# Performance work log

Hardware: AMD Instinct MI355X
Metric: run time of the kernel (lower is better)

The kernel has to match this reference:

```python
import jax, jax.numpy as jnp
import numpy as np

N, C, H, W = 64, 64, 128, 128
KH, KW = 3, 3


def setup_inputs() -> dict:
    key = jax.random.key(0)
    k1, k2 = jax.random.split(key)
    images = jax.random.normal(k1, (N, C, H, W), dtype=jnp.float32)
    kernels = jax.random.normal(k2, (N, C, KH, KW), dtype=jnp.float32)
    return {"images": images, "kernels": kernels}


def reference(images, kernels):
    # Per-sample conv: image i ([C,H,W]) convolved with kernel i ([C,kh,kw]) -> 1 channel.
    # Equivalent to a grouped conv with N groups:
    #   input  [1, N*C, H, W], weights [N, C, kh, kw], feature_group_count=N
    n, c, h, w = images.shape
    x = images.reshape(1, n * c, h, w)
    out = jax.lax.conv_general_dilated(
        x, kernels,
        window_strides=(1, 1),
        padding='VALID',
        dimension_numbers=('NCHW', 'OIHW', 'NCHW'),
        feature_group_count=n,
    )  # [1, N, H', W']
    return out.reshape(n, 1, out.shape[2], out.shape[3])
```

## Files before the change

kernel.cpp:

```cpp
#include <hip/hip_runtime.h>


#define NS   64
#define CCH  64
#define HH   128
#define WW   128
#define OHH  126
#define OWW  126
#define TH   16
#define IR   18
#define LDW  132
#define LDW4 33

__global__ __launch_bounds__(256, 2)
void ImageWiseConv2d_kernel(const float* __restrict__ img,
                            const float* __restrict__ ker,
                            float* __restrict__ out)
{
    __shared__ float buf[2][IR * LDW];

    const int tid = threadIdx.x;
    const int bx  = blockIdx.x;
    const int n   = bx >> 3;
    const int bt  = bx & 7;
    const int h0  = bt * TH;

    const int tx32 = tid & 31;
    const int rb   = tid >> 5;
    const float4* img4 = (const float4*)img;
    int gbase = (n * CCH) * (HH * WW / 4) + (h0 + rb) * (WW / 4) + tx32;
    const bool w2 = (rb < 2);
    const bool g2 = w2 && (h0 + rb + 16 < HH);
    const int lw0 = rb * LDW4 + tx32;

    const int tx = tid & 31;
    const int ty = tid >> 5;
    const int r0 = 2 * ty;
    const int c0 = 4 * tx;

    float acc0[4] = {0.f, 0.f, 0.f, 0.f};
    float acc1[4] = {0.f, 0.f, 0.f, 0.f};

    {
        float4 p0 = img4[gbase];
        float4 p1 = img4[gbase + 8 * (WW / 4)];
        float4 p2 = g2 ? img4[gbase + 16 * (WW / 4)] : make_float4(0.f, 0.f, 0.f, 0.f);
        float4* b0 = (float4*)buf[0];
        b0[lw0] = p0;
        b0[lw0 + 8 * LDW4] = p1;
        if (w2) b0[lw0 + 16 * LDW4] = p2;
    }
    __syncthreads();

    const float* __restrict__ kb = ker + (n * CCH) * 9;

    for (int c = 0; c < CCH; ++c) {
        float4 p0, p1, p2;
        const bool more = (c + 1 < CCH);
        if (more) {
            int gb = gbase + (c + 1) * (HH * WW / 4);
            p0 = img4[gb];
            p1 = img4[gb + 8 * (WW / 4)];
            p2 = g2 ? img4[gb + 16 * (WW / 4)] : make_float4(0.f, 0.f, 0.f, 0.f);
        }

        float w[9];
        #pragma unroll
        for (int q = 0; q < 9; ++q) w[q] = kb[c * 9 + q];

        const float* bc = buf[c & 1];
        float f[4][8];
        #pragma unroll
        for (int r = 0; r < 4; ++r) {
            float4 a  = *(const float4*)&bc[(r0 + r) * LDW + c0];
            float4 b2 = *(const float4*)&bc[(r0 + r) * LDW + c0 + 4];
            f[r][0] = a.x;  f[r][1] = a.y;  f[r][2] = a.z;  f[r][3] = a.w;
            f[r][4] = b2.x; f[r][5] = b2.y; f[r][6] = b2.z; f[r][7] = b2.w;
        }

        #pragma unroll
        for (int kh = 0; kh < 3; ++kh) {
            #pragma unroll
            for (int kw = 0; kw < 3; ++kw) {
                const float wv = w[kh * 3 + kw];
                #pragma unroll
                for (int j = 0; j < 4; ++j) {
                    acc0[j] = fmaf(wv, f[kh][j + kw], acc0[j]);
                    acc1[j] = fmaf(wv, f[kh + 1][j + kw], acc1[j]);
                }
            }
        }

        if (more) {
            float4* bn = (float4*)buf[(c + 1) & 1];
            bn[lw0] = p0;
            bn[lw0 + 8 * LDW4] = p1;
            if (w2) bn[lw0 + 16 * LDW4] = p2;
            __syncthreads();
        }
    }

    const int oh0 = h0 + r0;
    #pragma unroll
    for (int orow = 0; orow < 2; ++orow) {
        const int oh = oh0 + orow;
        if (oh < OHH) {
            float* op = out + (n * OHH + oh) * OWW + c0;
            const float* a = orow ? acc1 : acc0;
            #pragma unroll
            for (int j = 0; j < 4; ++j)
                if (c0 + j < OWW) op[j] = a[j];
        }
    }
}

extern "C" void kernel_launch(void* const* d_in, const int* in_sizes, int n_in,
                              void* d_out, int out_size, void* d_ws, size_t ws_size,
                              hipStream_t stream) {
    const float* img = (const float*)d_in[0];
    const float* ker = (const float*)d_in[1];
    float* out = (float*)d_out;

    dim3 grid(NS * 8);
    dim3 block(256);
    ImageWiseConv2d_kernel<<<grid, block, 0, stream>>>(img, ker, out);
}
```

Baseline: 358.1 us.

## Split channel reduction across four blocks with separate partial-sum reduce kernel

Splits the 64-channel accumulation into four groups of 16 channels, each handled by its own block, quadrupling the grid. Partial sums go to a padded workspace with vectorized stores, and a second kernel sums the four partials into the output. This aims to raise occupancy and memory-level parallelism for a latency-bound launch. It adds extra workspace traffic and a second kernel launch.

Measured after the change: 578.5 us. 1.62x slower.

```diff
diff --git a/kernel.cpp b/kernel.cpp
--- a/kernel.cpp
+++ b/kernel.cpp
@@ -11,24 +11,29 @@
 #define IR   18
 #define LDW  132
 #define LDW4 33
+#define NG   4
+#define CPG  16
+#define PSTR 128
 
-__global__ __launch_bounds__(256, 2)
-void ImageWiseConv2d_kernel(const float* __restrict__ img,
-                            const float* __restrict__ ker,
-                            float* __restrict__ out)
+__global__ __launch_bounds__(256, 4)
+void ImageWiseConv2d_main(const float* __restrict__ img,
+                          const float* __restrict__ ker,
+                          float* __restrict__ part)
 {
     __shared__ float buf[2][IR * LDW];
 
     const int tid = threadIdx.x;
     const int bx  = blockIdx.x;
-    const int n   = bx >> 3;
     const int bt  = bx & 7;
+    const int n   = (bx >> 3) & 63;
+    const int g   = bx >> 9;
     const int h0  = bt * TH;
 
     const int tx32 = tid & 31;
     const int rb   = tid >> 5;
     const float4* img4 = (const float4*)img;
-    int gbase = (n * CCH) * (HH * WW / 4) + (h0 + rb) * (WW / 4) + tx32;
+    const int chstride4 = HH * WW / 4;
+    int gbase = (n * CCH + g * CPG) * chstride4 + (h0 + rb) * (WW / 4) + tx32;
     const bool w2 = (rb < 2);
     const bool g2 = w2 && (h0 + rb + 16 < HH);
     const int lw0 = rb * LDW4 + tx32;
@@ -52,13 +57,13 @@
     }
     __syncthreads();
 
-    const float* __restrict__ kb = ker + (n * CCH) * 9;
+    const float* __restrict__ kb = ker + (n * CCH + g * CPG) * 9;
 
-    for (int c = 0; c < CCH; ++c) {
+    for (int c = 0; c < CPG; ++c) {
         float4 p0, p1, p2;
-        const bool more = (c + 1 < CCH);
+        const bool more = (c + 1 < CPG);
         if (more) {
-            int gb = gbase + (c + 1) * (HH * WW / 4);
+            int gb = gbase + (c + 1) * chstride4;
             p0 = img4[gb];
             p1 = img4[gb + 8 * (WW / 4)];
             p2 = g2 ? img4[gb + 16 * (WW / 4)] : make_float4(0.f, 0.f, 0.f, 0.f);
@@ -101,17 +106,36 @@
     }
 
     const int oh0 = h0 + r0;
-    #pragma unroll
-    for (int orow = 0; orow < 2; ++orow) {
-        const int oh = oh0 + orow;
+    {
+        const int oh = oh0;
         if (oh < OHH) {
-            float* op = out + (n * OHH + oh) * OWW + c0;
-            const float* a = orow ? acc1 : acc0;
-            #pragma unroll
-            for (int j = 0; j < 4; ++j)
-                if (c0 + j < OWW) op[j] = a[j];
+            float* pp = part + ((g * NS + n) * OHH + oh) * PSTR + c0;
+            *(float4*)pp = make_float4(acc0[0], acc0[1], acc0[2], acc0[3]);
         }
     }
+    {
+        const int oh = oh0 + 1;
+        if (oh < OHH) {
+            float* pp = part + ((g * NS + n) * OHH + oh) * PSTR + c0;
+            *(float4*)pp = make_float4(acc1[0], acc1[1], acc1[2], acc1[3]);
+        }
+    }
+}
+
+__global__ __launch_bounds__(256)
+void ImageWiseConv2d_reduce(const float* __restrict__ part,
+                            float* __restrict__ out)
+{
+    const int i = blockIdx.x * 256 + threadIdx.x;
+    const int total = NS * OHH * OWW;
+    if (i >= total) return;
+    const int n  = i / (OHH * OWW);
+    const int r  = i - n * (OHH * OWW);
+    const int oh = r / OWW;
+    const int ow = r - oh * OWW;
+    const int gs = NS * OHH * PSTR;
+    const int pb = (n * OHH + oh) * PSTR + ow;
+    out[i] = part[pb] + part[pb + gs] + part[pb + 2 * gs] + part[pb + 3 * gs];
 }
 
 extern "C" void kernel_launch(void* const* d_in, const int* in_sizes, int n_in,
@@ -119,9 +143,11 @@
                               hipStream_t stream) {
     const float* img = (const float*)d_in[0];
     const float* ker = (const float*)d_in[1];
-    float* out = (float*)d_out;
+    float* out  = (float*)d_out;
+    float* part = (float*)d_ws;
 
-    dim3 grid(NS * 8);
-    dim3 block(256);
-    ImageWiseConv2d_kernel<<<grid, block, 0, stream>>>(img, ker, out);
+    ImageWiseConv2d_main<<<dim3(NG * NS * 8), dim3(256), 0, stream>>>(img, ker, part);
+
+    const int total = NS * OHH * OWW;
+    ImageWiseConv2d_reduce<<<dim3((total + 255) / 256), dim3(256), 0, stream>>>(part, out);
 }
```

## Replace LDS-staged tiles with direct per-thread global loads and register prefetch

Applied to the files above, without the earlier changes.

Drops the double-buffered shared-memory tile and its per-channel barrier. Each thread now loads its own 4x6 input window straight from global memory, relying on L1/L2 to absorb the overlapping reads between neighbouring threads, and prefetches the next channel into registers. Output stores become float2 vectors. This removes LDS traffic and synchronisation, at the cost of redundant global/cache reads (each input element is fetched by several threads) and clamped row handling at the bottom edge.

Measured after the change: 356.7 us. About the same (-0.4%).

```diff
diff --git a/kernel.cpp b/kernel.cpp
--- a/kernel.cpp
+++ b/kernel.cpp
@@ -7,109 +7,115 @@
 #define WW   128
 #define OHH  126
 #define OWW  126
-#define TH   16
-#define IR   18
-#define LDW  132
-#define LDW4 33
+#define CHS  (HH * WW)
 
 __global__ __launch_bounds__(256, 2)
-void ImageWiseConv2d_kernel(const float* __restrict__ img,
+void ImageWiseConv2d_direct(const float* __restrict__ img,
                             const float* __restrict__ ker,
                             float* __restrict__ out)
 {
-    __shared__ float buf[2][IR * LDW];
-
     const int tid = threadIdx.x;
     const int bx  = blockIdx.x;
+    const int bt  = bx & 7;
     const int n   = bx >> 3;
-    const int bt  = bx & 7;
-    const int h0  = bt * TH;
+    const int h0  = bt * 16;
 
-    const int tx32 = tid & 31;
-    const int rb   = tid >> 5;
-    const float4* img4 = (const float4*)img;
-    int gbase = (n * CCH) * (HH * WW / 4) + (h0 + rb) * (WW / 4) + tx32;
-    const bool w2 = (rb < 2);
-    const bool g2 = w2 && (h0 + rb + 16 < HH);
-    const int lw0 = rb * LDW4 + tx32;
+    const int r0 = (tid >> 5) << 1;
+    const int c0 = (tid & 31) << 2;
 
-    const int tx = tid & 31;
-    const int ty = tid >> 5;
-    const int r0 = 2 * ty;
-    const int c0 = 4 * tx;
+    int ihr = h0 + r0;
+    if (ihr > HH - 4) ihr = HH - 4;
+    const int bOff = (c0 < 124) ? 4 : 2;
 
-    float acc0[4] = {0.f, 0.f, 0.f, 0.f};
-    float acc1[4] = {0.f, 0.f, 0.f, 0.f};
+    const float* p0 = img + (((n * CCH) * HH) + ihr) * WW + c0;
+    const float* kp = ker + (n * CCH) * 9;
 
-    {
-        float4 p0 = img4[gbase];
-        float4 p1 = img4[gbase + 8 * (WW / 4)];
-        float4 p2 = g2 ? img4[gbase + 16 * (WW / 4)] : make_float4(0.f, 0.f, 0.f, 0.f);
-        float4* b0 = (float4*)buf[0];
-        b0[lw0] = p0;
-        b0[lw0 + 8 * LDW4] = p1;
-        if (w2) b0[lw0 + 16 * LDW4] = p2;
-    }
-    __syncthreads();
+    float a00 = 0.f, a01 = 0.f, a02 = 0.f, a03 = 0.f;
+    float a10 = 0.f, a11 = 0.f, a12 = 0.f, a13 = 0.f;
 
-    const float* __restrict__ kb = ker + (n * CCH) * 9;
+    float4 A0, A1, A2, A3;
+    float2 B0, B1, B2, B3;
+    A0 = *(const float4*)(p0);
+    A1 = *(const float4*)(p0 + WW);
+    A2 = *(const float4*)(p0 + 2 * WW);
+    A3 = *(const float4*)(p0 + 3 * WW);
+    B0 = *(const float2*)(p0 + bOff);
+    B1 = *(const float2*)(p0 + WW + bOff);
+    B2 = *(const float2*)(p0 + 2 * WW + bOff);
+    B3 = *(const float2*)(p0 + 3 * WW + bOff);
 
     for (int c = 0; c < CCH; ++c) {
-        float4 p0, p1, p2;
+        float4 nA0, nA1, nA2, nA3;
+        float2 nB0, nB1, nB2, nB3;
         const bool more = (c + 1 < CCH);
         if (more) {
-            int gb = gbase + (c + 1) * (HH * WW / 4);
-            p0 = img4[gb];
-            p1 = img4[gb + 8 * (WW / 4)];
-            p2 = g2 ? img4[gb + 16 * (WW / 4)] : make_float4(0.f, 0.f, 0.f, 0.f);
+            const float* q = p0 + (c + 1) * CHS;
+            nA0 = *(const float4*)(q);
+            nA1 = *(const float4*)(q + WW);
+            nA2 = *(const float4*)(q + 2 * WW);
+            nA3 = *(const float4*)(q + 3 * WW);
+            nB0 = *(const float2*)(q + bOff);
+            nB1 = *(const float2*)(q + WW + bOff);
+            nB2 = *(const float2*)(q + 2 * WW + bOff);
+            nB3 = *(const float2*)(q + 3 * WW + bOff);
         }
 
-        float w[9];
-        #pragma unroll
-        for (int q = 0; q < 9; ++q) w[q] = kb[c * 9 + q];
+        const float w0 = kp[c * 9 + 0], w1 = kp[c * 9 + 1], w2 = kp[c * 9 + 2];
+        const float w3 = kp[c * 9 + 3], w4 = kp[c * 9 + 4], w5 = kp[c * 9 + 5];
+        const float w6 = kp[c * 9 + 6], w7 = kp[c * 9 + 7], w8 = kp[c * 9 + 8];
 
-        const float* bc = buf[c & 1];
-        float f[4][8];
-        #pragma unroll
-        for (int r = 0; r < 4; ++r) {
-            float4 a  = *(const float4*)&bc[(r0 + r) * LDW + c0];
-            float4 b2 = *(const float4*)&bc[(r0 + r) * LDW + c0 + 4];
-            f[r][0] = a.x;  f[r][1] = a.y;  f[r][2] = a.z;  f[r][3] = a.w;
-            f[r][4] = b2.x; f[r][5] = b2.y; f[r][6] = b2.z; f[r][7] = b2.w;
+        {
+            const float v0 = A0.x, v1 = A0.y, v2 = A0.z, v3 = A0.w, v4 = B0.x, v5 = B0.y;
+            a00 = fmaf(w0, v0, a00); a00 = fmaf(w1, v1, a00); a00 = fmaf(w2, v2, a00);
+            a01 = fmaf(w0, v1, a01); a01 = fmaf(w1, v2, a01); a01 = fmaf(w2, v3, a01);
+            a02 = fmaf(w0, v2, a02); a02 = fmaf(w1, v3, a02); a02 = fmaf(w2, v4, a02);
+            a03 = fmaf(w0, v3, a03); a03 = fmaf(w1, v4, a03); a03 = fmaf(w2, v5, a03);
         }
-
-        #pragma unroll
-        for (int kh = 0; kh < 3; ++kh) {
-            #pragma unroll
-            for (int kw = 0; kw < 3; ++kw) {
-                const float wv = w[kh * 3 + kw];
-                #pragma unroll
-                for (int j = 0; j < 4; ++j) {
-                    acc0[j] = fmaf(wv, f[kh][j + kw], acc0[j]);
-                    acc1[j] = fmaf(wv, f[kh + 1][j + kw], acc1[j]);
-                }
-            }
+        {
+            const float v0 = A1.x, v1 = A1.y, v2 = A1.z, v3 = A1.w, v4 = B1.x, v5 = B1.y;
+            a00 = fmaf(w3, v0, a00); a00 = fmaf(w4, v1, a00); a00 = fmaf(w5, v2, a00);
+            a01 = fmaf(w3, v1, a01); a01 = fmaf(w4, v2, a01); a01 = fmaf(w5, v3, a01);
+            a02 = fmaf(w3, v2, a02); a02 = fmaf(w4, v3, a02); a02 = fmaf(w5, v4, a02);
+            a03 = fmaf(w3, v3, a03); a03 = fmaf(w4, v4, a03); a03 = fmaf(w5, v5, a03);
+            a10 = fmaf(w0, v0, a10); a10 = fmaf(w1, v1, a10); a10 = fmaf(w2, v2, a10);
+            a11 = fmaf(w0, v1, a11); a11 = fmaf(w1, v2, a11); a11 = fmaf(w2, v3, a11);
+            a12 = fmaf(w0, v2, a12); a12 = fmaf(w1, v3, a12); a12 = fmaf(w2, v4, a12);
+            a13 = fmaf(w0, v3, a13); a13 = fmaf(w1, v4, a13); a13 = fmaf(w2, v5, a13);
+        }
+        {
+            const float v0 = A2.x, v1 = A2.y, v2 = A2.z, v3 = A2.w, v4 = B2.x, v5 = B2.y;
+            a00 = fmaf(w6, v0, a00); a00 = fmaf(w7, v1, a00); a00 = fmaf(w8, v2, a00);
+            a01 = fmaf(w6, v1, a01); a01 = fmaf(w7, v2, a01); a01 = fmaf(w8, v3, a01);
+            a02 = fmaf(w6, v2, a02); a02 = fmaf(w7, v3, a02); a02 = fmaf(w8, v4, a02);
+            a03 = fmaf(w6, v3, a03); a03 = fmaf(w7, v4, a03); a03 = fmaf(w8, v5, a03);
+            a10 = fmaf(w3, v0, a10); a10 = fmaf(w4, v1, a10); a10 = fmaf(w5, v2, a10);
+            a11 = fmaf(w3, v1, a11); a11 = fmaf(w4, v2, a11); a11 = fmaf(w5, v3, a11);
+            a12 = fmaf(w3, v2, a12); a12 = fmaf(w4, v3, a12); a12 = fmaf(w5, v4, a12);
+            a13 = fmaf(w3, v3, a13); a13 = fmaf(w4, v4, a13); a13 = fmaf(w5, v5, a13);
+        }
+        {
+            const float v0 = A3.x, v1 = A3.y, v2 = A3.z, v3 = A3.w, v4 = B3.x, v5 = B3.y;
+            a10 = fmaf(w6, v0, a10); a10 = fmaf(w7, v1, a10); a10 = fmaf(w8, v2, a10);
+            a11 = fmaf(w6, v1, a11); a11 = fmaf(w7, v2, a11); a11 = fmaf(w8, v3, a11);
+            a12 = fmaf(w6, v2, a12); a12 = fmaf(w7, v3, a12); a12 = fmaf(w8, v4, a12);
+            a13 = fmaf(w6, v3, a13); a13 = fmaf(w7, v4, a13); a13 = fmaf(w8, v5, a13);
         }
 
         if (more) {
-            float4* bn = (float4*)buf[(c + 1) & 1];
-            bn[lw0] = p0;
-            bn[lw0 + 8 * LDW4] = p1;
-            if (w2) bn[lw0 + 16 * LDW4] = p2;
-            __syncthreads();
+            A0 = nA0; A1 = nA1; A2 = nA2; A3 = nA3;
+            B0 = nB0; B1 = nB1; B2 = nB2; B3 = nB3;
         }
     }
 
     const int oh0 = h0 + r0;
-    #pragma unroll
-    for (int orow = 0; orow < 2; ++orow) {
-        const int oh = oh0 + orow;
-        if (oh < OHH) {
-            float* op = out + (n * OHH + oh) * OWW + c0;
-            const float* a = orow ? acc1 : acc0;
-            #pragma unroll
-            for (int j = 0; j < 4; ++j)
-                if (c0 + j < OWW) op[j] = a[j];
+    if (oh0 < OHH) {
+        float* o0 = out + (n * OHH + oh0) * OWW + c0;
+        float* o1 = o0 + OWW;
+        *(float2*)o0 = make_float2(a00, a01);
+        *(float2*)o1 = make_float2(a10, a11);
+        if (c0 < 124) {
+            *(float2*)(o0 + 2) = make_float2(a02, a03);
+            *(float2*)(o1 + 2) = make_float2(a12, a13);
         }
     }
 }
@@ -121,7 +127,5 @@
     const float* ker = (const float*)d_in[1];
     float* out = (float*)d_out;
 
-    dim3 grid(NS * 8);
-    dim3 block(256);
-    ImageWiseConv2d_kernel<<<grid, block, 0, stream>>>(img, ker, out);
+    ImageWiseConv2d_direct<<<dim3(NS * 8), dim3(256), 0, stream>>>(img, ker, out);
 }
```
